# Kernel optimization log

Measured on AMD Instinct MI355X. Metric: run time of the kernel, lower is better.

The kernel has to match this reference:

```python
import jax, jax.numpy as jnp
import numpy as np

D_MODEL, N_HEADS, N_KV, D_K = 4096, 32, 8, 128
N_REP = N_HEADS // N_KV  # n_kv_groups
SEQ = 2048
EPS = 1e-6


def _layernorm(x, gamma, beta):
    # LayerNorm over the last (d_k) axis
    mu = jnp.mean(x, axis=-1, keepdims=True)
    var = jnp.var(x, axis=-1, keepdims=True)
    return (x - mu) * jax.lax.rsqrt(var + EPS) * gamma + beta


def setup_inputs() -> dict:
    key = jax.random.key(0)
    ks = jax.random.split(key, 8)
    s = 0.02
    return {
        "x": jax.random.normal(ks[0], (1, SEQ, D_MODEL), jnp.float32),
        "k_cache": jnp.zeros((N_KV, SEQ, D_K), jnp.float32),
        "v_cache": jnp.zeros((N_KV, SEQ, D_K), jnp.float32),
        "Wq": jax.random.normal(ks[1], (N_HEADS * D_K, D_MODEL), jnp.float32) * s,
        "Wk": jax.random.normal(ks[2], (N_KV * D_K, D_MODEL), jnp.float32) * s,
        "Wv": jax.random.normal(ks[3], (N_KV * D_K, D_MODEL), jnp.float32) * s,
        "Wo": jax.random.normal(ks[4], (D_MODEL, D_MODEL), jnp.float32) * s,
        "q_gamma": jnp.ones((D_K,), jnp.float32),
        "q_beta": jnp.zeros((D_K,), jnp.float32),
        "k_gamma": jnp.ones((D_K,), jnp.float32),
        "k_beta": jnp.zeros((D_K,), jnp.float32),
        "positions": jnp.arange(SEQ, dtype=jnp.int32),
        "seq_id": 0,
    }


def reference(x, k_cache, v_cache, Wq, Wk, Wv, Wo, q_gamma, q_beta, k_gamma, k_beta, positions, seq_id):
    B, S, _ = x.shape
    # projections (no bias: attention_bias=False)
    q = (x @ Wq.T).reshape(B, S, N_HEADS, D_K)
    k = (x @ Wk.T).reshape(B, S, N_KV, D_K)
    v = (x @ Wv.T).reshape(B, S, N_KV, D_K)
    # per-head LayerNorm on d_k (q_norm / k_norm)
    q = _layernorm(q, q_gamma, q_beta)
    k = _layernorm(k, k_gamma, k_beta)
    # rotary in the source is identity (SimpleRotary returns x unchanged)
    # paged-cache update: scatter new K/V (batch 0) into cache at `positions`
    k_cache = k_cache.at[:, positions, :].set(jnp.swapaxes(k[0], 0, 1))  # [n_kv, S, d_k]
    v_cache = v_cache.at[:, positions, :].set(jnp.swapaxes(v[0], 0, 1))
    # gather cached KV up to max position (prefill: full SEQ, static for jit)
    K = k_cache[None, :, :S, :]  # [1, n_kv, S, d_k]
    V = v_cache[None, :, :S, :]
    # GQA repeat_kv: expand kv heads to n_heads
    K = jnp.repeat(K, N_REP, axis=1)  # [1, n_heads, S, d_k]
    V = jnp.repeat(V, N_REP, axis=1)
    Q = jnp.swapaxes(q, 1, 2)  # [B, n_heads, S, d_k]
    # causal SDPA (dropout_p=0 in eval)
    scores = jnp.einsum("bhqd,bhkd->bhqk", Q, K) / jnp.sqrt(jnp.float32(D_K))
    causal = jnp.tril(jnp.ones((S, S), dtype=bool))
    scores = jnp.where(causal, scores, jnp.finfo(scores.dtype).min)
    attn = jax.nn.softmax(scores, axis=-1)
    out = jnp.einsum("bhqk,bhkd->bhqd", attn, V)  # [B, n_heads, S, d_k]
    out = jnp.swapaxes(out, 1, 2).reshape(B, S, D_MODEL)
    return out @ Wo.T
```

## Files before the change

### kernel.cpp

```cpp
#include <hip/hip_runtime.h>
#include <stdint.h>

typedef short bf16x8 __attribute__((ext_vector_type(8)));
typedef float f32x4 __attribute__((ext_vector_type(4)));
typedef float f32x16 __attribute__((ext_vector_type(16)));

#define SEQ     2048
#define DM      4096
#define NQH     32
#define NKVH    8
#define DK      128
#define NQKV    6144

__device__ __forceinline__ unsigned short f2bfb(float f) {
    union { float f; unsigned u; } x; x.f = f;
    unsigned r = x.u + 0x7FFFu + ((x.u >> 16) & 1u);
    return (unsigned short)(r >> 16);
}

__device__ __forceinline__ unsigned cvt_pk_bf16(float a, float b) {
    unsigned r;
    asm("v_cvt_pk_bf16_f32 %0, %1, %2" : "=v"(r) : "v"(a), "v"(b));
    return r;
}

#if __has_builtin(__builtin_amdgcn_exp2f)
__device__ __forceinline__ float exp2_fast(float x) { return __builtin_amdgcn_exp2f(x); }
#else
__device__ __forceinline__ float exp2_fast(float x) { return exp2f(x); }
#endif

__device__ __forceinline__ void stage16(const void* g, void* l) {
    __builtin_amdgcn_global_load_lds(
        (const __attribute__((address_space(1))) void*)g,
        (__attribute__((address_space(3))) void*)l,
        16, 0, 0);
}

__global__ __launch_bounds__(256)
void cvt_bf16(const float4* __restrict__ src, ushort4* __restrict__ dst, int n4) {
    int i = blockIdx.x * 256 + threadIdx.x;
    const int stride = gridDim.x * 256;
    for (; i < n4; i += stride) {
        float4 f = src[i];
        ushort4 u;
        u.x = f2bfb(f.x); u.y = f2bfb(f.y); u.z = f2bfb(f.z); u.w = f2bfb(f.w);
        dst[i] = u;
    }
}

__global__ __launch_bounds__(256, 2)
void gemm_bt(const unsigned short* __restrict__ A, const unsigned short* __restrict__ B,
             float* __restrict__ C, int M, int N, int K)
{
    __shared__ __align__(16) unsigned short As[128 * 32];
    __shared__ __align__(16) unsigned short Bs[128 * 32];

    const int tid = threadIdx.x;
    const int w  = tid >> 6;
    const int l  = tid & 63;
    const int lr = l & 15;
    const int lg = l >> 4;
    const int m0 = blockIdx.y << 7;
    const int n0 = blockIdx.x << 7;
    const int wm = (w >> 1) << 6;
    const int wn = (w & 1) << 6;

    f32x4 acc[4][4];
#pragma unroll
    for (int i = 0; i < 4; ++i)
#pragma unroll
        for (int j = 0; j < 4; ++j) acc[i][j] = f32x4{0.f, 0.f, 0.f, 0.f};

    const int c0   = tid;
    const int row0 = c0 >> 2, kc0 = (c0 & 3) << 3;
    const int c1   = tid + 256;
    const int row1 = c1 >> 2, kc1 = (c1 & 3) << 3;
    const unsigned short* Ag = A + (size_t)m0 * K;
    const unsigned short* Bg = B + (size_t)n0 * K;
    char* AsB = (char*)As;
    char* BsB = (char*)Bs;
    const int wb = w << 10;

    const int nk = K >> 5;
    for (int kt = 0; kt < nk; ++kt) {
        const int ko = kt << 5;
        stage16(Ag + (size_t)row0 * K + ko + kc0, AsB + wb);
        stage16(Ag + (size_t)row1 * K + ko + kc1, AsB + 4096 + wb);
        stage16(Bg + (size_t)row0 * K + ko + kc0, BsB + wb);
        stage16(Bg + (size_t)row1 * K + ko + kc1, BsB + 4096 + wb);
        __syncthreads();

        bf16x8 af[4], bfr[4];
#pragma unroll
        for (int mi = 0; mi < 4; ++mi)
            af[mi] = *(const bf16x8*)(As + ((wm + (mi << 4) + lr) << 5) + (lg << 3));
#pragma unroll
        for (int ni = 0; ni < 4; ++ni)
            bfr[ni] = *(const bf16x8*)(Bs + ((wn + (ni << 4) + lr) << 5) + (lg << 3));
#pragma unroll
        for (int mi = 0; mi < 4; ++mi)
#pragma unroll
            for (int ni = 0; ni < 4; ++ni)
                acc[mi][ni] = __builtin_amdgcn_mfma_f32_16x16x32_bf16(af[mi], bfr[ni], acc[mi][ni], 0, 0, 0);
        __syncthreads();
    }

#pragma unroll
    for (int mi = 0; mi < 4; ++mi)
#pragma unroll
        for (int ni = 0; ni < 4; ++ni) {
            const int row = m0 + wm + (mi << 4) + (lg << 2);
            const int col = n0 + wn + (ni << 4) + lr;
            float* cp = C + (size_t)row * N + col;
#pragma unroll
            for (int r = 0; r < 4; ++r) cp[(size_t)r * N] = acc[mi][ni][r];
        }
}

__global__ __launch_bounds__(256)
void ln_qk(const float* __restrict__ Y,
           const float* __restrict__ qg, const float* __restrict__ qb,
           const float* __restrict__ kg, const float* __restrict__ kb,
           unsigned short* __restrict__ Q, unsigned short* __restrict__ Kc)
{
    const int seg = blockIdx.x * 4 + (threadIdx.x >> 6);
    const int l = threadIdx.x & 63;
    const int s = seg / 40;
    const int hh = seg - s * 40;

    const float* y = Y + (size_t)s * NQKV + hh * 128;
    float2 v = *(const float2*)(y + l * 2);
    float sum = v.x + v.y;
    float sq  = v.x * v.x + v.y * v.y;
#pragma unroll
    for (int d = 1; d < 64; d <<= 1) {
        sum += __shfl_xor(sum, d);
        sq  += __shfl_xor(sq, d);
    }
    const float mu  = sum * (1.f / 128.f);
    const float var = sq * (1.f / 128.f) - mu * mu;
    const float rs  = rsqrtf(var + 1e-6f);

    const float* g = (hh < 32) ? qg : kg;
    const float* b = (hh < 32) ? qb : kb;
    const float c = (hh < 32) ? (0.08838834764831845f * 1.4426950408889634f) : 1.0f;
    const float g0 = g[l * 2], g1 = g[l * 2 + 1];
    const float b0 = b[l * 2], b1 = b[l * 2 + 1];
    const unsigned short o0 = f2bfb(((v.x - mu) * rs * g0 + b0) * c);
    const unsigned short o1 = f2bfb(((v.y - mu) * rs * g1 + b1) * c);
    const unsigned pack = (unsigned)o0 | ((unsigned)o1 << 16);

    if (hh < 32) {
        unsigned* dst = (unsigned*)(Q + ((size_t)hh * SEQ + s) * 128 + l * 2);
        *dst = pack;
    } else {
        unsigned* dst = (unsigned*)(Kc + ((size_t)(hh - 32) * SEQ + s) * 128 + l * 2);
        *dst = pack;
    }
}

__global__ __launch_bounds__(256)
void v_transpose(const float* __restrict__ Y, unsigned short* __restrict__ Vt)
{
    __shared__ unsigned short t[64][132];
    const int h  = blockIdx.x;
    const int s0 = blockIdx.y << 6;
    const int tid = threadIdx.x;
    const float* y = Y + (size_t)s0 * NQKV + 5120 + h * 128;

#pragma unroll
    for (int p = 0; p < 16; ++p) {
        const int idx = p * 512 + tid * 2;
        const int s = idx >> 7, d = idx & 127;
        float2 v = *(const float2*)(y + (size_t)s * NQKV + d);
        t[s][d]     = f2bfb(v.x);
        t[s][d + 1] = f2bfb(v.y);
    }
    __syncthreads();
    unsigned short* out = Vt + (size_t)h * 128 * SEQ + s0;
#pragma unroll
    for (int p = 0; p < 16; ++p) {
        const int idx = p * 512 + tid * 2;
        const int d = idx >> 6, sp = idx & 63;
        unsigned pack = (unsigned)t[sp][d] | ((unsigned)t[sp + 1][d] << 16);
        *(unsigned*)(out + (size_t)d * SEQ + sp) = pack;
    }
}

__global__ __launch_bounds__(256, 2)
void attn(const unsigned short* __restrict__ Qb, const unsigned short* __restrict__ Kb,
          const unsigned short* __restrict__ Vt, unsigned short* __restrict__ Ob)
{
    const int h   = blockIdx.x;
    const int qt  = 15 - blockIdx.y;
    const int kvh = h >> 2;
    const int tid = threadIdx.x;
    const int w   = tid >> 6;
    const int l   = tid & 63;
    const int lq  = l & 31;
    const int hi  = l >> 5;
    const int q0  = qt << 7;
    const int wq  = q0 + (w << 5);
    const int qrow = wq + lq;

    const unsigned short* Qh = Qb + ((size_t)h * SEQ + wq) * 128;
    const unsigned short* Kh = Kb + (size_t)kvh * SEQ * 128;
    const unsigned short* Vh = Vt + (size_t)kvh * 128 * SEQ;

    bf16x8 qf[8];
#pragma unroll
    for (int ks = 0; ks < 8; ++ks)
        qf[ks] = *(const bf16x8*)(Qh + lq * 128 + ks * 16 + hi * 8);

    f32x16 o0_ = {0}, o1_ = {0}, o2_ = {0}, o3_ = {0};
    float m = -1.0e30f, lsum = 0.f;

    const int kv_end = wq + 32;

    for (int kv0 = 0; kv0 < kv_end; kv0 += 64) {
        f32x16 s0 = {0}, s1 = {0};
        const unsigned short* K0 = Kh + (size_t)kv0 * 128;
#pragma unroll
        for (int ks = 0; ks < 8; ++ks) {
            bf16x8 ka = *(const bf16x8*)(K0 + (size_t)lq * 128 + ks * 16 + hi * 8);
            bf16x8 kb2 = *(const bf16x8*)(K0 + (size_t)(32 + lq) * 128 + ks * 16 + hi * 8);
            s0 = __builtin_amdgcn_mfma_f32_32x32x16_bf16(ka, qf[ks], s0, 0, 0, 0);
            s1 = __builtin_amdgcn_mfma_f32_32x32x16_bf16(kb2, qf[ks], s1, 0, 0, 0);
        }

        if (kv0 + 63 > wq) {
#pragma unroll
            for (int r = 0; r < 16; ++r) {
                const int kvl = (r & 3) + 8 * (r >> 2) + 4 * hi;
                if (kv0 + kvl > qrow)      s0[r] = -1.0e30f;
                if (kv0 + 32 + kvl > qrow) s1[r] = -1.0e30f;
            }
        }

        float pm = s0[0];
#pragma unroll
        for (int r = 1; r < 16; ++r) pm = fmaxf(pm, s0[r]);
#pragma unroll
        for (int r = 0; r < 16; ++r) pm = fmaxf(pm, s1[r]);
        pm = fmaxf(pm, __shfl_xor(pm, 32));

        if (!__all(pm - m <= 8.0f)) {
            const float mn = fmaxf(m, pm);
            const float al = exp2_fast(m - mn);
            lsum *= al;
#pragma unroll
            for (int r = 0; r < 16; ++r) { o0_[r] *= al; o1_[r] *= al; o2_[r] *= al; o3_[r] *= al; }
            m = mn;
        }

        float rs = 0.f;
#pragma unroll
        for (int r = 0; r < 16; ++r) { s0[r] = exp2_fast(s0[r] - m); rs += s0[r]; }
#pragma unroll
        for (int r = 0; r < 16; ++r) { s1[r] = exp2_fast(s1[r] - m); rs += s1[r]; }
        rs += __shfl_xor(rs, 32);
        lsum += rs;

        unsigned pw0[2][4], pw1[2][4];
#pragma unroll
        for (int u = 0; u < 4; ++u) {
            pw0[0][u] = cvt_pk_bf16(s0[u * 4 + 0], s0[u * 4 + 1]);
            pw1[0][u] = cvt_pk_bf16(s0[u * 4 + 2], s0[u * 4 + 3]);
            pw0[1][u] = cvt_pk_bf16(s1[u * 4 + 0], s1[u * 4 + 1]);
            pw1[1][u] = cvt_pk_bf16(s1[u * 4 + 2], s1[u * 4 + 3]);
        }

#pragma unroll
        for (int ksg = 0; ksg < 4; ++ksg) {
            const int b  = ksg >> 1;
            const int ks = ksg & 1;
            const unsigned a0 = pw0[b][2 * ks],     a1 = pw1[b][2 * ks];
            const unsigned b0 = pw0[b][2 * ks + 1], b1 = pw1[b][2 * ks + 1];
            const unsigned sa0 = __shfl_xor(a0, 32);
            const unsigned sb0 = __shfl_xor(b0, 32);
            const unsigned sa1 = __shfl_xor(a1, 32);
            const unsigned sb1 = __shfl_xor(b1, 32);
            union { unsigned wrd[4]; bf16x8 v; } pb;
            pb.wrd[0] = hi ? sb0 : a0;
            pb.wrd[1] = hi ? sb1 : a1;
            pb.wrd[2] = hi ? b0  : sa0;
            pb.wrd[3] = hi ? b1  : sa1;

            const unsigned short* Vk = Vh + kv0 + 16 * ksg + 8 * hi;
            {
                bf16x8 vf0 = *(const bf16x8*)(Vk + (size_t)(lq) * SEQ);
                o0_ = __builtin_amdgcn_mfma_f32_32x32x16_bf16(vf0, pb.v, o0_, 0, 0, 0);
                bf16x8 vf1 = *(const bf16x8*)(Vk + (size_t)(32 + lq) * SEQ);
                o1_ = __builtin_amdgcn_mfma_f32_32x32x16_bf16(vf1, pb.v, o1_, 0, 0, 0);
                bf16x8 vf2 = *(const bf16x8*)(Vk + (size_t)(64 + lq) * SEQ);
                o2_ = __builtin_amdgcn_mfma_f32_32x32x16_bf16(vf2, pb.v, o2_, 0, 0, 0);
                bf16x8 vf3 = *(const bf16x8*)(Vk + (size_t)(96 + lq) * SEQ);
                o3_ = __builtin_amdgcn_mfma_f32_32x32x16_bf16(vf3, pb.v, o3_, 0, 0, 0);
            }
        }
    }

    const float inv = 1.0f / lsum;
    unsigned short* orow = Ob + (size_t)qrow * DM + h * 128;
#pragma unroll
    for (int r = 0; r < 16; r += 2) {
        const int doff = 8 * (r >> 2) + 4 * hi + (r & 3);
        *(unsigned*)(orow + 0  + doff) = cvt_pk_bf16(o0_[r] * inv, o0_[r + 1] * inv);
        *(unsigned*)(orow + 32 + doff) = cvt_pk_bf16(o1_[r] * inv, o1_[r + 1] * inv);
        *(unsigned*)(orow + 64 + doff) = cvt_pk_bf16(o2_[r] * inv, o2_[r + 1] * inv);
        *(unsigned*)(orow + 96 + doff) = cvt_pk_bf16(o3_[r] * inv, o3_[r + 1] * inv);
    }
}

extern "C" void kernel_launch(void* const* d_in, const int* in_sizes, int n_in,
                              void* d_out, int out_size, void* d_ws, size_t ws_size,
                              hipStream_t stream)
{
    const float* x  = (const float*)d_in[0];
    const float* Wq = (const float*)d_in[3];
    const float* Wk = (const float*)d_in[4];
    const float* Wv = (const float*)d_in[5];
    const float* Wo = (const float*)d_in[6];
    const float* qg = (const float*)d_in[7];
    const float* qb = (const float*)d_in[8];
    const float* kg = (const float*)d_in[9];
    const float* kb = (const float*)d_in[10];
    float* out = (float*)d_out;

    char* ws = (char*)d_ws;
    unsigned short* xb   = (unsigned short*)(ws);
    unsigned short* wqkv = (unsigned short*)(ws + 16777216);
    unsigned short* wo   = (unsigned short*)(ws + 67108864);
    float*          y    = (float*)        (ws + 100663296);
    unsigned short* qbuf = (unsigned short*)(ws + 150994944);
    unsigned short* kbuf = (unsigned short*)(ws + 167772160);
    unsigned short* vtb  = (unsigned short*)(ws + 171966464);
    unsigned short* ob   = (unsigned short*)(ws + 176160768);

    {
        int n4 = (SEQ * DM) / 4;
        cvt_bf16<<<2048, 256, 0, stream>>>((const float4*)x, (ushort4*)xb, n4);
        n4 = (NQH * DK * DM) / 4;
        cvt_bf16<<<2048, 256, 0, stream>>>((const float4*)Wq, (ushort4*)wqkv, n4);
        n4 = (NKVH * DK * DM) / 4;
        cvt_bf16<<<2048, 256, 0, stream>>>((const float4*)Wk, (ushort4*)(wqkv + 16777216), n4);
        cvt_bf16<<<2048, 256, 0, stream>>>((const float4*)Wv, (ushort4*)(wqkv + 20971520), n4);
        n4 = (DM * DM) / 4;
        cvt_bf16<<<2048, 256, 0, stream>>>((const float4*)Wo, (ushort4*)wo, n4);
    }

    gemm_bt<<<dim3(NQKV / 128, SEQ / 128), 256, 0, stream>>>(xb, wqkv, y, SEQ, NQKV, DM);

    ln_qk<<<(SEQ * 40) / 4, 256, 0, stream>>>(y, qg, qb, kg, kb, qbuf, kbuf);

    v_transpose<<<dim3(NKVH, SEQ / 64), 256, 0, stream>>>(y, vtb);

    attn<<<dim3(NQH, SEQ / 128), 256, 0, stream>>>(qbuf, kbuf, vtb, ob);

    gemm_bt<<<dim3(DM / 128, SEQ / 128), 256, 0, stream>>>(ob, wo, out, SEQ, DM, DM);
}
```

Before: 641.6 us.

## Stage K/V tiles in double-buffered swizzled LDS shared across attention waves

The attention kernel now loads each 64-row K tile and the matching V tile into shared memory once per block, using a stage16 helper, instead of every wave reading K and V straight from global memory. Two LDS buffers let the next tile's loads run while the current tile is computed, and an XOR swizzle on the column index is meant to avoid bank conflicts on the fragment reads. The loop also adds s_setprio around the MFMA groups and turns the row max/sum reductions into trees. This costs 64KB of LDS per block and a block-wide barrier every tile, which can lower occupancy and make waves that skip a masked tile wait anyway.

```diff
diff --git a/kernel.cpp b/kernel.cpp
--- a/kernel.cpp
+++ b/kernel.cpp
@@ -192,6 +192,9 @@
 void attn(const unsigned short* __restrict__ Qb, const unsigned short* __restrict__ Kb,
           const unsigned short* __restrict__ Vt, unsigned short* __restrict__ Ob)
 {
+    __shared__ __align__(16) unsigned short Kl[2][64 * 128];
+    __shared__ __align__(16) unsigned short Vl[2][128 * 64];
+
     const int h   = blockIdx.x;
     const int qt  = 15 - blockIdx.y;
     const int kvh = h >> 2;
@@ -208,6 +211,17 @@
     const unsigned short* Kh = Kb + (size_t)kvh * SEQ * 128;
     const unsigned short* Vh = Vt + (size_t)kvh * 128 * SEQ;
 
+    int koff[4], voff[4];
+#pragma unroll
+    for (int p = 0; p < 4; ++p) {
+        const int c  = p * 256 + tid;
+        const int kr = c >> 4, kc = c & 15;
+        koff[p] = kr * 128 + ((kc ^ (kr & 7)) << 3);
+        const int vr = c >> 3, vc = c & 7;
+        voff[p] = vr * SEQ + ((vc ^ (vr & 7)) << 3);
+    }
+    const int dstb = w << 10;
+
     bf16x8 qf[8];
 #pragma unroll
     for (int ks = 0; ks < 8; ++ks)
@@ -216,89 +230,133 @@
     f32x16 o0_ = {0}, o1_ = {0}, o2_ = {0}, o3_ = {0};
     float m = -1.0e30f, lsum = 0.f;
 
-    const int kv_end = wq + 32;
-
-    for (int kv0 = 0; kv0 < kv_end; kv0 += 64) {
-        f32x16 s0 = {0}, s1 = {0};
-        const unsigned short* K0 = Kh + (size_t)kv0 * 128;
-#pragma unroll
-        for (int ks = 0; ks < 8; ++ks) {
-            bf16x8 ka = *(const bf16x8*)(K0 + (size_t)lq * 128 + ks * 16 + hi * 8);
-            bf16x8 kb2 = *(const bf16x8*)(K0 + (size_t)(32 + lq) * 128 + ks * 16 + hi * 8);
-            s0 = __builtin_amdgcn_mfma_f32_32x32x16_bf16(ka, qf[ks], s0, 0, 0, 0);
-            s1 = __builtin_amdgcn_mfma_f32_32x32x16_bf16(kb2, qf[ks], s1, 0, 0, 0);
+    const int nt = (q0 + 128) >> 6;
+    const int sw = (lq & 7) << 4;
+
+#pragma unroll
+    for (int p = 0; p < 4; ++p)
+        stage16(Kh + koff[p], (char*)Kl[0] + p * 4096 + dstb);
+#pragma unroll
+    for (int p = 0; p < 4; ++p)
+        stage16(Vh + voff[p], (char*)Vl[0] + p * 4096 + dstb);
+    __syncthreads();
+
+    int buf = 0;
+    for (int t = 0; t < nt; ++t) {
+        const int kv0 = t << 6;
+
+        if (t + 1 < nt) {
+            const int kvn = kv0 + 64;
+#pragma unroll
+            for (int p = 0; p < 4; ++p)
+                stage16(Kh + (size_t)kvn * 128 + koff[p], (char*)(Kl[buf ^ 1]) + p * 4096 + dstb);
+#pragma unroll
+            for (int p = 0; p < 4; ++p)
+                stage16(Vh + kvn + voff[p], (char*)(Vl[buf ^ 1]) + p * 4096 + dstb);
         }
 
-        if (kv0 + 63 > wq) {
-#pragma unroll
-            for (int r = 0; r < 16; ++r) {
-                const int kvl = (r & 3) + 8 * (r >> 2) + 4 * hi;
-                if (kv0 + kvl > qrow)      s0[r] = -1.0e30f;
-                if (kv0 + 32 + kvl > qrow) s1[r] = -1.0e30f;
+        if (kv0 <= wq + 31) {
+            const char* Kb0 = (const char*)(Kl[buf]) + lq * 256;
+            const char* Kb1 = (const char*)(Kl[buf]) + (lq + 32) * 256;
+            bf16x8 kf0[8], kf1[8];
+#pragma unroll
+            for (int ks = 0; ks < 8; ++ks) {
+                const int cb = (ks * 32 + hi * 16) ^ sw;
+                kf0[ks] = *(const bf16x8*)(Kb0 + cb);
+                kf1[ks] = *(const bf16x8*)(Kb1 + cb);
+            }
+            f32x16 s0 = {0}, s1 = {0};
+            __builtin_amdgcn_s_setprio(1);
+#pragma unroll
+            for (int ks = 0; ks < 8; ++ks) {
+                s0 = __builtin_amdgcn_mfma_f32_32x32x16_bf16(kf0[ks], qf[ks], s0, 0, 0, 0);
+                s1 = __builtin_amdgcn_mfma_f32_32x32x16_bf16(kf1[ks], qf[ks], s1, 0, 0, 0);
+            }
+            __builtin_amdgcn_s_setprio(0);
+
+            if (kv0 + 63 > wq) {
+#pragma unroll
+                for (int r = 0; r < 16; ++r) {
+                    const int kvl = (r & 3) + 8 * (r >> 2) + 4 * hi;
+                    if (kv0 + kvl > qrow)      s0[r] = -1.0e30f;
+                    if (kv0 + 32 + kvl > qrow) s1[r] = -1.0e30f;
+                }
+            }
+
+            float m8[8];
+#pragma unroll
+            for (int i = 0; i < 8; ++i)
+                m8[i] = fmaxf(fmaxf(s0[i], s0[i + 8]), fmaxf(s1[i], s1[i + 8]));
+#pragma unroll
+            for (int i = 0; i < 4; ++i) m8[i] = fmaxf(m8[i], m8[i + 4]);
+            float pm = fmaxf(fmaxf(m8[0], m8[1]), fmaxf(m8[2], m8[3]));
+            pm = fmaxf(pm, __shfl_xor(pm, 32));
+
+            if (!__all(pm - m <= 8.0f)) {
+                const float mn = fmaxf(m, pm);
+                const float al = exp2_fast(m - mn);
+                lsum *= al;
+#pragma unroll
+                for (int r = 0; r < 16; ++r) { o0_[r] *= al; o1_[r] *= al; o2_[r] *= al; o3_[r] *= al; }
+                m = mn;
+            }
+
+#pragma unroll
+            for (int r = 0; r < 16; ++r) s0[r] = exp2_fast(s0[r] - m);
+#pragma unroll
+            for (int r = 0; r < 16; ++r) s1[r] = exp2_fast(s1[r] - m);
+            float a8[8];
+#pragma unroll
+            for (int i = 0; i < 8; ++i)
+                a8[i] = (s0[i] + s0[i + 8]) + (s1[i] + s1[i + 8]);
+#pragma unroll
+            for (int i = 0; i < 4; ++i) a8[i] += a8[i + 4];
+            float rs = (a8[0] + a8[1]) + (a8[2] + a8[3]);
+            rs += __shfl_xor(rs, 32);
+            lsum += rs;
+
+            unsigned pw0[2][4], pw1[2][4];
+#pragma unroll
+            for (int u = 0; u < 4; ++u) {
+                pw0[0][u] = cvt_pk_bf16(s0[u * 4 + 0], s0[u * 4 + 1]);
+                pw1[0][u] = cvt_pk_bf16(s0[u * 4 + 2], s0[u * 4 + 3]);
+                pw0[1][u] = cvt_pk_bf16(s1[u * 4 + 0], s1[u * 4 + 1]);
+                pw1[1][u] = cvt_pk_bf16(s1[u * 4 + 2], s1[u * 4 + 3]);
+            }
+
+            const char* Vb = (const char*)(Vl[buf]);
+#pragma unroll
+            for (int ksg = 0; ksg < 4; ++ksg) {
+                const int b  = ksg >> 1;
+                const int ks = ksg & 1;
+                const unsigned a0 = pw0[b][2 * ks],     a1 = pw1[b][2 * ks];
+                const unsigned b0 = pw0[b][2 * ks + 1], b1 = pw1[b][2 * ks + 1];
+                const unsigned sa0 = __shfl_xor(a0, 32);
+                const unsigned sb0 = __shfl_xor(b0, 32);
+                const unsigned sa1 = __shfl_xor(a1, 32);
+                const unsigned sb1 = __shfl_xor(b1, 32);
+                union { unsigned wrd[4]; bf16x8 v; } pb;
+                pb.wrd[0] = hi ? sb0 : a0;
+                pb.wrd[1] = hi ? sb1 : a1;
+                pb.wrd[2] = hi ? b0  : sa0;
+                pb.wrd[3] = hi ? b1  : sa1;
+
+                const int cb = (ksg * 32 + hi * 16) ^ sw;
+                bf16x8 vf0 = *(const bf16x8*)(Vb + (lq)       * 128 + cb);
+                bf16x8 vf1 = *(const bf16x8*)(Vb + (lq + 32)  * 128 + cb);
+                bf16x8 vf2 = *(const bf16x8*)(Vb + (lq + 64)  * 128 + cb);
+                bf16x8 vf3 = *(const bf16x8*)(Vb + (lq + 96)  * 128 + cb);
+                __builtin_amdgcn_s_setprio(1);
+                o0_ = __builtin_amdgcn_mfma_f32_32x32x16_bf16(vf0, pb.v, o0_, 0, 0, 0);
+                o1_ = __builtin_amdgcn_mfma_f32_32x32x16_bf16(vf1, pb.v, o1_, 0, 0, 0);
+                o2_ = __builtin_amdgcn_mfma_f32_32x32x16_bf16(vf2, pb.v, o2_, 0, 0, 0);
+                o3_ = __builtin_amdgcn_mfma_f32_32x32x16_bf16(vf3, pb.v, o3_, 0, 0, 0);
+                __builtin_amdgcn_s_setprio(0);
             }
         }
 
-        float pm = s0[0];
-#pragma unroll
-        for (int r = 1; r < 16; ++r) pm = fmaxf(pm, s0[r]);
-#pragma unroll
-        for (int r = 0; r < 16; ++r) pm = fmaxf(pm, s1[r]);
-        pm = fmaxf(pm, __shfl_xor(pm, 32));
-
-        if (!__all(pm - m <= 8.0f)) {
-            const float mn = fmaxf(m, pm);
-            const float al = exp2_fast(m - mn);
-            lsum *= al;
-#pragma unroll
-            for (int r = 0; r < 16; ++r) { o0_[r] *= al; o1_[r] *= al; o2_[r] *= al; o3_[r] *= al; }
-            m = mn;
-        }
-
-        float rs = 0.f;
-#pragma unroll
-        for (int r = 0; r < 16; ++r) { s0[r] = exp2_fast(s0[r] - m); rs += s0[r]; }
-#pragma unroll
-        for (int r = 0; r < 16; ++r) { s1[r] = exp2_fast(s1[r] - m); rs += s1[r]; }
-        rs += __shfl_xor(rs, 32);
-        lsum += rs;
-
-        unsigned pw0[2][4], pw1[2][4];
-#pragma unroll
-        for (int u = 0; u < 4; ++u) {
-            pw0[0][u] = cvt_pk_bf16(s0[u * 4 + 0], s0[u * 4 + 1]);
-            pw1[0][u] = cvt_pk_bf16(s0[u * 4 + 2], s0[u * 4 + 3]);
-            pw0[1][u] = cvt_pk_bf16(s1[u * 4 + 0], s1[u * 4 + 1]);
-            pw1[1][u] = cvt_pk_bf16(s1[u * 4 + 2], s1[u * 4 + 3]);
-        }
-
-#pragma unroll
-        for (int ksg = 0; ksg < 4; ++ksg) {
-            const int b  = ksg >> 1;
-            const int ks = ksg & 1;
-            const unsigned a0 = pw0[b][2 * ks],     a1 = pw1[b][2 * ks];
-            const unsigned b0 = pw0[b][2 * ks + 1], b1 = pw1[b][2 * ks + 1];
-            const unsigned sa0 = __shfl_xor(a0, 32);
-            const unsigned sb0 = __shfl_xor(b0, 32);
-            const unsigned sa1 = __shfl_xor(a1, 32);
-            const unsigned sb1 = __shfl_xor(b1, 32);
-            union { unsigned wrd[4]; bf16x8 v; } pb;
-            pb.wrd[0] = hi ? sb0 : a0;
-            pb.wrd[1] = hi ? sb1 : a1;
-            pb.wrd[2] = hi ? b0  : sa0;
-            pb.wrd[3] = hi ? b1  : sa1;
-
-            const unsigned short* Vk = Vh + kv0 + 16 * ksg + 8 * hi;
-            {
-                bf16x8 vf0 = *(const bf16x8*)(Vk + (size_t)(lq) * SEQ);
-                o0_ = __builtin_amdgcn_mfma_f32_32x32x16_bf16(vf0, pb.v, o0_, 0, 0, 0);
-                bf16x8 vf1 = *(const bf16x8*)(Vk + (size_t)(32 + lq) * SEQ);
-                o1_ = __builtin_amdgcn_mfma_f32_32x32x16_bf16(vf1, pb.v, o1_, 0, 0, 0);
-                bf16x8 vf2 = *(const bf16x8*)(Vk + (size_t)(64 + lq) * SEQ);
-                o2_ = __builtin_amdgcn_mfma_f32_32x32x16_bf16(vf2, pb.v, o2_, 0, 0, 0);
-                bf16x8 vf3 = *(const bf16x8*)(Vk + (size_t)(96 + lq) * SEQ);
-                o3_ = __builtin_amdgcn_mfma_f32_32x32x16_bf16(vf3, pb.v, o3_, 0, 0, 0);
-            }
-        }
+        __syncthreads();
+        buf ^= 1;
     }
 
     const float inv = 1.0f / lsum;
```

Result: faster. 527.9 us (-17.7%).
